# Kernel tuning notes

Measured on AMD Instinct MI355X. Metric: run time of the kernel, lower is better.

Reference implementation:

```python
import jax, jax.numpy as jnp
import numpy as np

LSH_BUCKETS = 32
LSH_BANDWIDTH = 2.0
N_HASHES = 4
K_MAX = 64


def setup_inputs() -> dict:
    key0 = jax.random.key(0)
    kq, kk, kw = jax.random.split(key0, 3)
    B, L, D = 4, 4096, 64
    query = jax.random.normal(kq, (B, L, D), dtype=jnp.float32)
    key = jax.random.normal(kk, (B, L, D), dtype=jnp.float32)
    # learned LSH projection: maps binary features (D) -> N_HASHES hash values
    W = jax.random.normal(kw, (D, N_HASHES), dtype=jnp.float32)
    return {"query": query, "key": key, "W": W, "head_idx": 0}


def _lsh_hash(x_bin, W):
    # standard E2LSH-style hash: floor(<x, w> / bandwidth) mod n_buckets
    proj = x_bin @ W  # (B, L, N_HASHES)
    return jnp.floor(proj / LSH_BANDWIDTH).astype(jnp.int32) % LSH_BUCKETS


def reference(query, key, W, head_idx):
    B, L, _ = query.shape
    # binary_quantize: (x > 0).float()
    q_bin = (query > 0).astype(query.dtype)
    k_bin = (key > 0).astype(key.dtype)
    qh = _lsh_hash(q_bin, W)  # (B, L, N_HASHES) ints in [0, LSH_BUCKETS)
    kh = _lsh_hash(k_bin, W)
    # pack the N_HASHES hash values into one integer code per token;
    # codes equal  <=>  all hash values equal (values are in [0, LSH_BUCKETS))
    radix = (LSH_BUCKETS ** jnp.arange(N_HASHES)).astype(jnp.int32)  # (N_HASHES,)
    q_code = jnp.sum(qh * radix, axis=-1)  # (B, L)
    k_code = jnp.sum(kh * radix, axis=-1)  # (B, L)
    # match[b, i, j] = all hashes of query i equal hashes of key j
    match = q_code[:, :, None] == k_code[:, None, :]  # (B, L, L) bool
    # collect first K_MAX matching j per (b, i), pad with -1 (matches the
    # sequential early-break loop since j is scanned in increasing order)
    j_idx = jnp.arange(L, dtype=jnp.int32)
    score = jnp.where(match, j_idx[None, None, :], L)  # non-matches pushed to end
    first = jnp.sort(score, axis=-1)[:, :, :K_MAX]      # (B, L, K_MAX)
    candidates = jnp.where(first < L, first, -1)        # int32 indices, -1 pad
    return candidates
```

## Files before the change

### kernel.cpp

```cpp
#include <hip/hip_runtime.h>

#define KMAX 64
#define BB 4
#define LL 4096
#define DD 64
#define TOK (BB * LL)
#define QPW 4

typedef unsigned long long u64;

__global__ __launch_bounds__(64) void codes_kernel(
        const float* __restrict__ q,
        const float* __restrict__ k,
        const float* __restrict__ W,
        int* __restrict__ codes ) {
    __shared__ float sW[DD * 4];
    int lane = threadIdx.x;
    #pragma unroll
    for (int i = 0; i < 4; ++i) sW[i * 64 + lane] = W[i * 64 + lane];
    __syncthreads();

    int u = blockIdx.x * 64 + lane;
    const float* src = (u < TOK) ? q : k;
    int t = u & (TOK - 1);

    const float4* xp = (const float4*)(src + (size_t)t * DD);
    float4 x[16];
    #pragma unroll
    for (int i = 0; i < 16; ++i) x[i] = xp[i];

    float p0 = 0.f, p1 = 0.f, p2 = 0.f, p3 = 0.f;
    const float4* wrow = (const float4*)sW;
    #pragma unroll
    for (int d = 0; d < DD; ++d) {
        float xv = ((const float*)x)[d];
        float b = (xv > 0.f) ? 1.0f : 0.0f;
        float4 w = wrow[d];
        p0 = fmaf(b, w.x, p0);
        p1 = fmaf(b, w.y, p1);
        p2 = fmaf(b, w.z, p2);
        p3 = fmaf(b, w.w, p3);
    }
    int h0 = ((int)floorf(p0 * 0.5f)) & 31;
    int h1 = ((int)floorf(p1 * 0.5f)) & 31;
    int h2 = ((int)floorf(p2 * 0.5f)) & 31;
    int h3 = ((int)floorf(p3 * 0.5f)) & 31;
    codes[u] = h0 | (h1 << 5) | (h2 << 10) | (h3 << 15);
}

__global__ __launch_bounds__(256) void find_kernel(
        const int* __restrict__ qcodes,
        const int* __restrict__ kcodes,
        int* __restrict__ out) {
    __shared__ int skc[LL];
    int tid = threadIdx.x;
    int blk = blockIdx.x;
    int b = blk >> 8;

    const int4* src = (const int4*)(kcodes + b * LL);
    int4* dst = (int4*)skc;
    #pragma unroll
    for (int i = 0; i < 4; ++i) dst[tid + i * 256] = src[tid + i * 256];
    __syncthreads();

    int wave = blk * 4 + (tid >> 6);
    int lane = tid & 63;
    int qbase = wave * QPW;
    const int* qp = qcodes + qbase;
    int* outb = out + (size_t)qbase * KMAX;
    u64 lowmask = (1ull << lane) - 1ull;

    const int4* skc4 = (const int4*)skc;
    int4 kv[16];
    #pragma unroll
    for (int g = 0; g < 16; ++g) kv[g] = skc4[g * 64 + lane];

    int qc[QPW], cnt[QPW];
    #pragma unroll
    for (int i = 0; i < QPW; ++i) { qc[i] = qp[i]; cnt[i] = 0; }

    #pragma unroll
    for (int g = 0; g < 16; ++g) {
        bool a0 = (kv[g].x == qc[0]) | (kv[g].y == qc[0]) | (kv[g].z == qc[0]) | (kv[g].w == qc[0]);
        bool a1 = (kv[g].x == qc[1]) | (kv[g].y == qc[1]) | (kv[g].z == qc[1]) | (kv[g].w == qc[1]);
        bool a2 = (kv[g].x == qc[2]) | (kv[g].y == qc[2]) | (kv[g].z == qc[2]) | (kv[g].w == qc[2]);
        bool a3 = (kv[g].x == qc[3]) | (kv[g].y == qc[3]) | (kv[g].z == qc[3]) | (kv[g].w == qc[3]);
        if (__ballot(a0 | a1 | a2 | a3) == 0) continue;
        int j0 = g * 256 + lane * 4;
        #pragma unroll
        for (int i = 0; i < QPW; ++i) {
            if (cnt[i] >= KMAX) continue;
            bool m0 = (kv[g].x == qc[i]), m1 = (kv[g].y == qc[i]);
            bool m2 = (kv[g].z == qc[i]), m3 = (kv[g].w == qc[i]);
            if (__ballot(m0 | m1 | m2 | m3) == 0) continue;
            u64 b0 = __ballot(m0), b1 = __ballot(m1);
            u64 b2 = __ballot(m2), b3 = __ballot(m3);
            int before = __popcll(b0 & lowmask) + __popcll(b1 & lowmask)
                       + __popcll(b2 & lowmask) + __popcll(b3 & lowmask);
            int pos = cnt[i] + before;
            int* op = outb + i * KMAX;
            if (m0) { if (pos < KMAX) op[pos] = j0;     ++pos; }
            if (m1) { if (pos < KMAX) op[pos] = j0 + 1; ++pos; }
            if (m2) { if (pos < KMAX) op[pos] = j0 + 2; ++pos; }
            if (m3) { if (pos < KMAX) op[pos] = j0 + 3; ++pos; }
            cnt[i] += __popcll(b0) + __popcll(b1) + __popcll(b2) + __popcll(b3);
        }
    }
    #pragma unroll
    for (int i = 0; i < QPW; ++i) {
        int p = cnt[i] + lane;
        if (p < KMAX) outb[i * KMAX + p] = -1;
    }
}

extern "C" void kernel_launch(void* const* d_in, const int* in_sizes, int n_in,
                              void* d_out, int out_size, void* d_ws, size_t ws_size,
                              hipStream_t stream) {
    const float* q = (const float*)d_in[0];
    const float* k = (const float*)d_in[1];
    const float* W = (const float*)d_in[2];
    int* out = (int*)d_out;
    int* codes = (int*)d_ws;
    int* qcodes = codes;
    int* kcodes = codes + TOK;

    codes_kernel<<<(2 * TOK) / 64, 64, 0, stream>>>(q, k, W, codes);

    find_kernel<<<TOK / (QPW * 4), 256, 0, stream>>>(qcodes, kcodes, out);
}
```

Measured before the change: 20.35 us.

## Fuse query hash computation into the candidate-finding kernel

The query code computation moves out of the first kernel and into the find kernel. Each block stages its 16 query rows in padded shared memory and hashes them with 16 threads before the matching scan. The first kernel now processes only keys, which halves its grid and drops the query-code round trip through global memory. In exchange, every find block pays a serialized 16-thread hash stage and an extra barrier, which delays the scan.

Result: slower. 22.27 us (+9.4%).

```diff
diff --git a/kernel.cpp b/kernel.cpp
--- a/kernel.cpp
+++ b/kernel.cpp
@@ -6,25 +6,22 @@
 #define DD 64
 #define TOK (BB * LL)
 #define QPW 4
+#define QPB 16
 
 typedef unsigned long long u64;
 
-__global__ __launch_bounds__(64) void codes_kernel(
-        const float* __restrict__ q,
+__global__ __launch_bounds__(64) void kcodes_kernel(
         const float* __restrict__ k,
         const float* __restrict__ W,
-        int* __restrict__ codes ) {
+        int* __restrict__ kcodes ) {
     __shared__ float sW[DD * 4];
     int lane = threadIdx.x;
     #pragma unroll
     for (int i = 0; i < 4; ++i) sW[i * 64 + lane] = W[i * 64 + lane];
     __syncthreads();
 
-    int u = blockIdx.x * 64 + lane;
-    const float* src = (u < TOK) ? q : k;
-    int t = u & (TOK - 1);
-
-    const float4* xp = (const float4*)(src + (size_t)t * DD);
+    int t = blockIdx.x * 64 + lane;
+    const float4* xp = (const float4*)(k + (size_t)t * DD);
     float4 x[16];
     #pragma unroll
     for (int i = 0; i < 16; ++i) x[i] = xp[i];
@@ -45,28 +42,63 @@
     int h1 = ((int)floorf(p1 * 0.5f)) & 31;
     int h2 = ((int)floorf(p2 * 0.5f)) & 31;
     int h3 = ((int)floorf(p3 * 0.5f)) & 31;
-    codes[u] = h0 | (h1 << 5) | (h2 << 10) | (h3 << 15);
+    kcodes[t] = h0 | (h1 << 5) | (h2 << 10) | (h3 << 15);
 }
 
 __global__ __launch_bounds__(256) void find_kernel(
-        const int* __restrict__ qcodes,
+        const float* __restrict__ q,
+        const float* __restrict__ W,
         const int* __restrict__ kcodes,
         int* __restrict__ out) {
-    __shared__ int skc[LL];
+    __shared__ float sW[DD * 4];
+    __shared__ int   skc[LL];
+    __shared__ float sq[QPB * 65];
+    __shared__ int   sqc[QPB];
     int tid = threadIdx.x;
     int blk = blockIdx.x;
     int b = blk >> 8;
+    int qb0 = blk * QPB;
 
-    const int4* src = (const int4*)(kcodes + b * LL);
+    sW[tid] = W[tid];
+
+    const int4* ksrc = (const int4*)(kcodes + b * LL);
     int4* dst = (int4*)skc;
     #pragma unroll
-    for (int i = 0; i < 4; ++i) dst[tid + i * 256] = src[tid + i * 256];
+    for (int i = 0; i < 4; ++i) dst[tid + i * 256] = ksrc[tid + i * 256];
+
+    {
+        const float4* qsrc = (const float4*)(q + (size_t)qb0 * DD);
+        float4 f = qsrc[tid];
+        int row = tid >> 4, c4 = (tid & 15) * 4;
+        float* r = sq + row * 65 + c4;
+        r[0] = f.x; r[1] = f.y; r[2] = f.z; r[3] = f.w;
+    }
     __syncthreads();
 
-    int wave = blk * 4 + (tid >> 6);
-    int lane = tid & 63;
-    int qbase = wave * QPW;
-    const int* qp = qcodes + qbase;
+    if (tid < QPB) {
+        const float* xr = sq + tid * 65;
+        const float4* wrow = (const float4*)sW;
+        float p0 = 0.f, p1 = 0.f, p2 = 0.f, p3 = 0.f;
+        #pragma unroll
+        for (int d = 0; d < DD; ++d) {
+            float xv = xr[d];
+            float bq = (xv > 0.f) ? 1.0f : 0.0f;
+            float4 w = wrow[d];
+            p0 = fmaf(bq, w.x, p0);
+            p1 = fmaf(bq, w.y, p1);
+            p2 = fmaf(bq, w.z, p2);
+            p3 = fmaf(bq, w.w, p3);
+        }
+        int h0 = ((int)floorf(p0 * 0.5f)) & 31;
+        int h1 = ((int)floorf(p1 * 0.5f)) & 31;
+        int h2 = ((int)floorf(p2 * 0.5f)) & 31;
+        int h3 = ((int)floorf(p3 * 0.5f)) & 31;
+        sqc[tid] = h0 | (h1 << 5) | (h2 << 10) | (h3 << 15);
+    }
+    __syncthreads();
+
+    int wave = tid >> 6, lane = tid & 63;
+    int qbase = qb0 + wave * QPW;
     int* outb = out + (size_t)qbase * KMAX;
     u64 lowmask = (1ull << lane) - 1ull;
 
@@ -77,7 +109,7 @@
 
     int qc[QPW], cnt[QPW];
     #pragma unroll
-    for (int i = 0; i < QPW; ++i) { qc[i] = qp[i]; cnt[i] = 0; }
+    for (int i = 0; i < QPW; ++i) { qc[i] = sqc[wave * QPW + i]; cnt[i] = 0; }
 
     #pragma unroll
     for (int g = 0; g < 16; ++g) {
@@ -120,11 +152,9 @@
     const float* k = (const float*)d_in[1];
     const float* W = (const float*)d_in[2];
     int* out = (int*)d_out;
-    int* codes = (int*)d_ws;
-    int* qcodes = codes;
-    int* kcodes = codes + TOK;
+    int* kcodes = (int*)d_ws;
 
-    codes_kernel<<<(2 * TOK) / 64, 64, 0, stream>>>(q, k, W, codes);
+    kcodes_kernel<<<TOK / 64, 64, 0, stream>>>(k, W, kcodes);
 
-    find_kernel<<<TOK / (QPW * 4), 256, 0, stream>>>(qcodes, kcodes, out);
+    find_kernel<<<TOK / QPB, 256, 0, stream>>>(q, W, kcodes, out);
 }
```
